# Performance work log

Hardware: AMD Instinct MI355X
Metric: run time of the kernel (lower is better)

The kernel has to match this reference:

```python
import jax, jax.numpy as jnp
import numpy as np

B, N, P, DIM, H = 8, 1024, 77, 1024, 16
HD = DIM // H
LN_EPS = 1e-5


def setup_inputs() -> dict:
    key = jax.random.key(0)
    ks = jax.random.split(key, 8)
    s = 0.02  # weight init scale
    return {
        "x": jax.random.normal(ks[0], (B, N, DIM), jnp.float32),
        "x_text": jax.random.normal(ks[1], (B, P, DIM), jnp.float32),
        "Wq": jax.random.normal(ks[2], (DIM, DIM), jnp.float32) * s,
        "Wk": jax.random.normal(ks[3], (DIM, DIM), jnp.float32) * s,
        "Wv": jax.random.normal(ks[4], (DIM, DIM), jnp.float32) * s,
        "gate": jax.random.normal(ks[5], (1, H, 1, 1), jnp.float32) * 0.5,
        "ln_g": jnp.ones((DIM,), jnp.float32),
        "ln_b": jnp.zeros((DIM,), jnp.float32),
        "Wp": jax.random.normal(ks[6], (DIM, DIM), jnp.float32) * s,
        "bp": jnp.zeros((DIM,), jnp.float32),
    }


def reference(x, x_text, Wq, Wk, Wv, gate, ln_g, ln_b, Wp, bp):
    b, n, c = x.shape
    h = gate.shape[1]
    # subln projections; prefix text tokens are concatenated onto k/v (not q)
    q = x @ Wq.T                                             # [B,N,C]
    k = jnp.concatenate([x_text @ Wk.T, x @ Wk.T], axis=1)   # [B,P+N,C]
    v = jnp.concatenate([x_text @ Wv.T, x @ Wv.T], axis=1)   # [B,P+N,C]
    kv = k.shape[1]
    q = q.reshape(b, n, h, -1).transpose(0, 2, 1, 3)         # [B,H,N,d]
    k = k.reshape(b, kv, h, -1).transpose(0, 2, 1, 3)        # [B,H,K,d]
    v = v.reshape(b, kv, h, -1).transpose(0, 2, 1, 3)        # [B,H,K,d]
    d = q.shape[-1]
    scores = jnp.einsum('bhnd,bhkd->bhnk', q, k) / jnp.sqrt(jnp.float32(d))
    # gated split softmax: first key column is softmaxed alone (== 1) and gated
    first = jnp.tanh(gate) * jnp.ones_like(scores[..., :1])  # [B,H,N,1]
    rest = jax.nn.softmax(scores[..., 1:], axis=-1)          # [B,H,N,K-1]
    attn = jnp.concatenate([first, rest], axis=-1)           # [B,H,N,K]
    out = jnp.einsum('bhnk,bhkd->bhnd', attn, v)             # AV reduce
    out = out.transpose(0, 2, 1, 3).reshape(b, n, -1)        # [B,N,C]
    # original casts to bfloat16 then back to LN weight dtype
    out = out.astype(jnp.bfloat16).astype(jnp.float32)
    mu = jnp.mean(out, axis=-1, keepdims=True)
    var = jnp.var(out, axis=-1, keepdims=True)
    out = (out - mu) / jnp.sqrt(var + LN_EPS) * ln_g + ln_b
    return out @ Wp.T + bp
```

## Files before the change

kernel.cpp:

```cpp
#include <hip/hip_runtime.h>
#include <stdint.h>

#define DIM   1024
#define NB    8
#define NSEQ  1024
#define NP    77
#define NH    16
#define NKVR  1104
#define KVP   1104
#define QSCALE 0.18033688011112042f

typedef short          bf16x8 __attribute__((ext_vector_type(8)));
typedef float          f32x4  __attribute__((ext_vector_type(4)));
typedef float          f32x16 __attribute__((ext_vector_type(16)));
typedef unsigned short u16x8  __attribute__((ext_vector_type(8)));
typedef unsigned short u16x4  __attribute__((ext_vector_type(4)));
typedef unsigned int   u32x4  __attribute__((ext_vector_type(4)));

__device__ __forceinline__ float bf2f(unsigned short h) {
  return __uint_as_float(((unsigned int)h) << 16);
}
__device__ __forceinline__ unsigned short f2bf(float f) {
  unsigned int u = __float_as_uint(f);
  unsigned int r = u + 0x7FFFu + ((u >> 16) & 1u);
  return (unsigned short)(r >> 16);
}
__device__ __forceinline__ unsigned int cvt_pk_bf16(float lo, float hi) {
  unsigned int r;
  asm volatile("v_cvt_pk_bf16_f32 %0, %1, %2" : "=v"(r) : "v"(lo), "v"(hi));
  return r;
}

__global__ __launch_bounds__(256) void cast_kernel(const float* __restrict__ in,
                                                   unsigned short* __restrict__ out,
                                                   int n4, float scale) {
  int i = blockIdx.x * 256 + threadIdx.x;
  if (i >= n4) return;
  float4 v = reinterpret_cast<const float4*>(in)[i];
  u16x4 o;
  o[0] = f2bf(v.x * scale); o[1] = f2bf(v.y * scale);
  o[2] = f2bf(v.z * scale); o[3] = f2bf(v.w * scale);
  reinterpret_cast<u16x4*>(out)[i] = o;
}

__global__ __launch_bounds__(256) void cast_x_kernel(const float* __restrict__ in,
                                                     unsigned short* __restrict__ xkv) {
  int i = blockIdx.x * 256 + threadIdx.x;
  if (i >= (NB * NSEQ * DIM) / 4) return;
  const int e    = i * 4;
  const int row  = e >> 10;
  const int cin  = e & 1023;
  const int batch = row >> 10;
  const int r     = row & 1023;
  float4 v = *reinterpret_cast<const float4*>(in + (size_t)e);
  u16x4 o;
  o[0] = f2bf(v.x); o[1] = f2bf(v.y); o[2] = f2bf(v.z); o[3] = f2bf(v.w);
  *reinterpret_cast<u16x4*>(xkv + (size_t)(batch * NKVR + 80 + r) * DIM + cin) = o;
}

__global__ __launch_bounds__(256) void cast_xt_kernel(const float* __restrict__ in,
                                                      unsigned short* __restrict__ xkv) {
  int i = blockIdx.x * 256 + threadIdx.x;
  if (i >= (NB * NP * DIM) / 4) return;
  const int e    = i * 4;
  const int row  = e >> 10;
  const int cin  = e & 1023;
  const int batch = row / NP;
  const int r     = row - batch * NP;
  float4 v = *reinterpret_cast<const float4*>(in + (size_t)e);
  u16x4 o;
  o[0] = f2bf(v.x); o[1] = f2bf(v.y); o[2] = f2bf(v.z); o[3] = f2bf(v.w);
  *reinterpret_cast<u16x4*>(xkv + (size_t)(batch * NKVR + r) * DIM + cin) = o;
}

__global__ __launch_bounds__(256) void zero_hole_kernel(unsigned short* __restrict__ xkv) {
  int i = blockIdx.x * 256 + threadIdx.x;
  if (i >= (NB * 3 * DIM) / 4) return;
  const int e    = i * 4;
  const int row  = e >> 10;
  const int cin  = e & 1023;
  const int batch = row / 3;
  const int hr    = row - batch * 3;
  u16x4 z = {0, 0, 0, 0};
  *reinterpret_cast<u16x4*>(xkv + (size_t)(batch * NKVR + 77 + hr) * DIM + cin) = z;
}

__device__ __forceinline__ void gload_lds16(const void* g, void* l) {
  __builtin_amdgcn_global_load_lds(
      (const __attribute__((address_space(1))) void*)g,
      (__attribute__((address_space(3))) void*)l, 16, 0, 0);
}

__global__ __launch_bounds__(256) void gemm_qkv(
    const unsigned short* __restrict__ A, const unsigned short* __restrict__ B,
    unsigned short* __restrict__ Qo, unsigned short* __restrict__ Ko,
    unsigned short* __restrict__ Vto) {
  __shared__ __align__(16) unsigned short As[128 * 32];
  __shared__ __align__(16) unsigned short Bs[128 * 32];
  const int id   = blockIdx.x;
  const int sid  = (id & 7) * 207 + (id >> 3);
  const int bx   = sid / 24;
  const int by   = sid - bx * 24;
  const int m0   = bx * 128;
  const int n0   = by * 128;
  const int t    = threadIdx.x;
  const int w    = t >> 6;
  const int lane = t & 63;
  const int wr   = w >> 1, wc = w & 1;
  const int lr   = lane & 15;
  const int k0   = (lane >> 4) * 8;

  f32x4 acc[4][4];
#pragma unroll
  for (int i = 0; i < 4; ++i)
#pragma unroll
    for (int j = 0; j < 4; ++j) acc[i][j] = f32x4{0.f, 0.f, 0.f, 0.f};

  for (int kt = 0; kt < 32; ++kt) {
#pragma unroll
    for (int p = 0; p < 2; ++p) {
      const int c   = p * 256 + t;
      const int row = c >> 2;
      const int cid = c & 3;
      gload_lds16(A + (size_t)(m0 + row) * DIM + kt * 32 + cid * 8,
                  (char*)As + p * 4096 + w * 1024);
      gload_lds16(B + (size_t)(n0 + row) * DIM + kt * 32 + cid * 8,
                  (char*)Bs + p * 4096 + w * 1024);
    }
    __syncthreads();
    bf16x8 af[4], bfr[4];
#pragma unroll
    for (int mi = 0; mi < 4; ++mi)
      af[mi] = *reinterpret_cast<const bf16x8*>(As + (wr * 64 + mi * 16 + lr) * 32 + k0);
#pragma unroll
    for (int ni = 0; ni < 4; ++ni)
      bfr[ni] = *reinterpret_cast<const bf16x8*>(Bs + (wc * 64 + ni * 16 + lr) * 32 + k0);
#pragma unroll
    for (int mi = 0; mi < 4; ++mi)
#pragma unroll
      for (int ni = 0; ni < 4; ++ni)
        acc[mi][ni] = __builtin_amdgcn_mfma_f32_16x16x32_bf16(af[mi], bfr[ni], acc[mi][ni], 0, 0, 0);
    __syncthreads();
  }

  const int rq  = lane >> 4;
  const int seg = n0 >> 10;
  if (seg == 0) {
#pragma unroll
    for (int mi = 0; mi < 4; ++mi) {
#pragma unroll
      for (int i = 0; i < 4; ++i) {
        const int m     = m0 + wr * 64 + mi * 16 + rq * 4 + i;
        const int batch = m / NKVR;
        const int kv    = m - batch * NKVR;
        if (kv < 80) continue;
        const size_t qrow = (size_t)batch * NSEQ + (kv - 80);
#pragma unroll
        for (int ni = 0; ni < 4; ++ni) {
          const int col = n0 + wc * 64 + ni * 16 + lr;
          Qo[qrow * DIM + col] = f2bf(acc[mi][ni][i]);
        }
      }
    }
  } else if (seg == 1) {
#pragma unroll
    for (int mi = 0; mi < 4; ++mi) {
#pragma unroll
      for (int i = 0; i < 4; ++i) {
        const int m = m0 + wr * 64 + mi * 16 + rq * 4 + i;
#pragma unroll
        for (int ni = 0; ni < 4; ++ni) {
          const int col = n0 + wc * 64 + ni * 16 + lr - 1024;
          Ko[(size_t)m * DIM + col] = f2bf(acc[mi][ni][i]);
        }
      }
    }
  } else {
#pragma unroll
    for (int mi = 0; mi < 4; ++mi) {
      const int mb    = m0 + wr * 64 + mi * 16 + rq * 4;
      const int batch = mb / NKVR;
      const int kv    = mb - batch * NKVR;
#pragma unroll
      for (int ni = 0; ni < 4; ++ni) {
        const int col = n0 + wc * 64 + ni * 16 + lr - 2048;
        const int hh = col >> 6, dd = col & 63;
        u16x4 o;
        o[0] = f2bf(acc[mi][ni][0]); o[1] = f2bf(acc[mi][ni][1]);
        o[2] = f2bf(acc[mi][ni][2]); o[3] = f2bf(acc[mi][ni][3]);
        *reinterpret_cast<u16x4*>(Vto +
            ((size_t)((batch * NH + hh) * 64 + dd)) * KVP + kv) = o;
      }
    }
  }
}

__global__ __launch_bounds__(256) void gemm_out(
    const unsigned short* __restrict__ A, const unsigned short* __restrict__ B,
    float* __restrict__ C, const float* __restrict__ bias) {
  __shared__ __align__(16) unsigned short As[128 * 32];
  __shared__ __align__(16) unsigned short Bs[128 * 32];
  const int t    = threadIdx.x;
  const int w    = t >> 6;
  const int lane = t & 63;
  const int m0   = blockIdx.x * 128;
  const int n0   = blockIdx.y * 128;
  const int wr   = w >> 1, wc = w & 1;
  const int lr   = lane & 15;
  const int k0   = (lane >> 4) * 8;

  f32x4 acc[4][4];
#pragma unroll
  for (int i = 0; i < 4; ++i)
#pragma unroll
    for (int j = 0; j < 4; ++j) acc[i][j] = f32x4{0.f, 0.f, 0.f, 0.f};

  for (int kt = 0; kt < 32; ++kt) {
#pragma unroll
    for (int p = 0; p < 2; ++p) {
      const int c   = p * 256 + t;
      const int row = c >> 2;
      const int cid = c & 3;
      gload_lds16(A + (size_t)(m0 + row) * DIM + kt * 32 + cid * 8,
                  (char*)As + p * 4096 + w * 1024);
      gload_lds16(B + (size_t)(n0 + row) * DIM + kt * 32 + cid * 8,
                  (char*)Bs + p * 4096 + w * 1024);
    }
    __syncthreads();
    bf16x8 af[4], bfr[4];
#pragma unroll
    for (int mi = 0; mi < 4; ++mi)
      af[mi] = *reinterpret_cast<const bf16x8*>(As + (wr * 64 + mi * 16 + lr) * 32 + k0);
#pragma unroll
    for (int ni = 0; ni < 4; ++ni)
      bfr[ni] = *reinterpret_cast<const bf16x8*>(Bs + (wc * 64 + ni * 16 + lr) * 32 + k0);
#pragma unroll
    for (int mi = 0; mi < 4; ++mi)
#pragma unroll
      for (int ni = 0; ni < 4; ++ni)
        acc[mi][ni] = __builtin_amdgcn_mfma_f32_16x16x32_bf16(af[mi], bfr[ni], acc[mi][ni], 0, 0, 0);
    __syncthreads();
  }

  const int rq = lane >> 4;
#pragma unroll
  for (int mi = 0; mi < 4; ++mi) {
#pragma unroll
    for (int i = 0; i < 4; ++i) {
      const int m = m0 + wr * 64 + mi * 16 + rq * 4 + i;
#pragma unroll
      for (int ni = 0; ni < 4; ++ni) {
        const int col = n0 + wc * 64 + ni * 16 + lr;
        C[(size_t)m * DIM + col] = acc[mi][ni][i] + bias[col];
      }
    }
  }
}

__global__ __launch_bounds__(128, 4) void attn_mfma(
    const unsigned short* __restrict__ Q, const unsigned short* __restrict__ K,
    const unsigned short* __restrict__ Vt, const float* __restrict__ gate,
    unsigned short* __restrict__ O) {
  const int wid  = threadIdx.x >> 6;
  const int lane = threadIdx.x & 63;
  const int ql   = lane & 31;
  const int hi   = lane >> 5;
  const int bh   = blockIdx.x;
  const int b    = bh >> 4;
  const int h    = bh & 15;
  const int q0   = blockIdx.y * 64 + wid * 32;

  __shared__ float v0f[2][64];

  const unsigned short* Vtbase = Vt + ((size_t)((b * NH + h) * 64)) * KVP;
  const unsigned short* Kbase  = K  + ((size_t)b * NKVR) * DIM + h * 64 + hi * 8;

  v0f[wid][lane] = bf2f(Vtbase[(size_t)lane * KVP]);

  bf16x8 bq[4];
  const unsigned short* Qrow = Q + ((size_t)(b * NSEQ + q0 + ql)) * DIM + h * 64 + hi * 8;
#pragma unroll
  for (int j = 0; j < 4; ++j)
    bq[j] = *reinterpret_cast<const bf16x8*>(Qrow + j * 16);

  f32x16 o0, o1;
#pragma unroll
  for (int r = 0; r < 16; ++r) { o0[r] = 0.f; o1[r] = 0.f; }
  float lsum = 0.f;

  auto kblock = [&](int kbase, int mm) {
    int krow = kbase + ql;
    if (mm == 3) krow = krow < NKVR ? krow : (NKVR - 1);
    const unsigned short* kr = Kbase + (size_t)krow * DIM;
    bf16x8 ak[4];
#pragma unroll
    for (int j = 0; j < 4; ++j)
      ak[j] = *reinterpret_cast<const bf16x8*>(kr + j * 16);

    f32x16 s;
#pragma unroll
    for (int r = 0; r < 16; ++r) s[r] = 0.f;
#pragma unroll
    for (int j = 0; j < 4; ++j)
      s = __builtin_amdgcn_mfma_f32_32x32x16_bf16(ak[j], bq[j], s, 0, 0, 0);

    bf16x8 av[2][2];
#pragma unroll
    for (int ss = 0; ss < 2; ++ss) {
      if (mm == 3 && ss == 1) continue;
      const int kv = kbase + ss * 16 + hi * 8;
#pragma unroll
      for (int n = 0; n < 2; ++n)
        av[ss][n] = *reinterpret_cast<const bf16x8*>(
            Vtbase + (size_t)(n * 32 + ql) * KVP + kv);
    }

    if (mm == 1) {
      if (hi == 0) s[0] = -1.0e30f;
    } else if (mm == 2) {
      if (hi == 1) { s[5] = -1.0e30f; s[6] = -1.0e30f; s[7] = -1.0e30f; }
    } else if (mm == 3) {
#pragma unroll
      for (int r = 8; r < 16; ++r) s[r] = -1.0e30f;
    }

    float ts = 0.f;
#pragma unroll
    for (int r = 0; r < 16; ++r) { s[r] = __builtin_exp2f(s[r]); ts += s[r]; }
    lsum += ts;

#pragma unroll
    for (int ss = 0; ss < 2; ++ss) {
      if (mm == 3 && ss == 1) continue;
      const int R = 8 * ss;
      const unsigned int p0 = cvt_pk_bf16(s[R + 0], s[R + 1]);
      const unsigned int p1 = cvt_pk_bf16(s[R + 2], s[R + 3]);
      const unsigned int p2 = cvt_pk_bf16(s[R + 4], s[R + 5]);
      const unsigned int p3 = cvt_pk_bf16(s[R + 6], s[R + 7]);
      const unsigned int t0 = (unsigned int)__shfl_xor((int)p0, 32);
      const unsigned int t1 = (unsigned int)__shfl_xor((int)p1, 32);
      const unsigned int t2 = (unsigned int)__shfl_xor((int)p2, 32);
      const unsigned int t3 = (unsigned int)__shfl_xor((int)p3, 32);
      u32x4 wv;
      wv[0] = hi ? t2 : p0;
      wv[1] = hi ? t3 : p1;
      wv[2] = hi ? p2 : t0;
      wv[3] = hi ? p3 : t1;
      const bf16x8 bp = __builtin_bit_cast(bf16x8, wv);
      o0 = __builtin_amdgcn_mfma_f32_32x32x16_bf16(av[ss][0], bp, o0, 0, 0, 0);
      o1 = __builtin_amdgcn_mfma_f32_32x32x16_bf16(av[ss][1], bp, o1, 0, 0, 0);
    }
  };

  kblock(0, 1);
  kblock(32, 0);
  kblock(64, 2);
  kblock(96, 0);
  for (int t = 2; t < 17; ++t) {
    kblock(t * 64, 0);
    kblock(t * 64 + 32, 0);
  }
  kblock(1088, 3);

  const float lt  = lsum + __shfl_xor(lsum, 32);
  const float inv = 1.f / lt;
  const float gv  = tanhf(gate[h]);
  unsigned short* Orow = O + ((size_t)(b * NSEQ + q0 + ql)) * DIM + h * 64;
#pragma unroll
  for (int n = 0; n < 2; ++n) {
#pragma unroll
    for (int g = 0; g < 4; ++g) {
      const int d0 = n * 32 + 8 * g + 4 * hi;
      const float4 vv = *reinterpret_cast<const float4*>(&v0f[wid][d0]);
      float e0, e1, e2, e3;
      if (n == 0) {
        e0 = o0[4 * g + 0]; e1 = o0[4 * g + 1]; e2 = o0[4 * g + 2]; e3 = o0[4 * g + 3];
      } else {
        e0 = o1[4 * g + 0]; e1 = o1[4 * g + 1]; e2 = o1[4 * g + 2]; e3 = o1[4 * g + 3];
      }
      u16x4 ov;
      ov[0] = f2bf(e0 * inv + gv * vv.x);
      ov[1] = f2bf(e1 * inv + gv * vv.y);
      ov[2] = f2bf(e2 * inv + gv * vv.z);
      ov[3] = f2bf(e3 * inv + gv * vv.w);
      *reinterpret_cast<u16x4*>(Orow + d0) = ov;
    }
  }
}

__global__ __launch_bounds__(256) void ln_kernel(const unsigned short* __restrict__ in,
                                                 const float* __restrict__ g,
                                                 const float* __restrict__ beta,
                                                 unsigned short* __restrict__ out) {
  const int row = blockIdx.x;
  const int t   = threadIdx.x;
  const u16x4 hv = *reinterpret_cast<const u16x4*>(in + (size_t)row * DIM + t * 4);
  const float v0 = bf2f(hv[0]), v1 = bf2f(hv[1]), v2 = bf2f(hv[2]), v3 = bf2f(hv[3]);
  float sum = v0 + v1 + v2 + v3;
  float sq  = v0 * v0 + v1 * v1 + v2 * v2 + v3 * v3;
  for (int off = 32; off; off >>= 1) {
    sum += __shfl_xor(sum, off);
    sq  += __shfl_xor(sq, off);
  }
  __shared__ float red[8];
  if ((t & 63) == 0) { red[t >> 6] = sum; red[4 + (t >> 6)] = sq; }
  __syncthreads();
  sum = red[0] + red[1] + red[2] + red[3];
  sq  = red[4] + red[5] + red[6] + red[7];
  const float mu  = sum * (1.f / DIM);
  const float var = sq * (1.f / DIM) - mu * mu;
  const float rs  = 1.f / sqrtf(var + 1e-5f);
  const float4 gv = *reinterpret_cast<const float4*>(g + t * 4);
  const float4 bv = *reinterpret_cast<const float4*>(beta + t * 4);
  u16x4 o;
  o[0] = f2bf((v0 - mu) * rs * gv.x + bv.x);
  o[1] = f2bf((v1 - mu) * rs * gv.y + bv.y);
  o[2] = f2bf((v2 - mu) * rs * gv.z + bv.z);
  o[3] = f2bf((v3 - mu) * rs * gv.w + bv.w);
  *reinterpret_cast<u16x4*>(out + (size_t)row * DIM + t * 4) = o;
}

extern "C" void kernel_launch(void* const* d_in, const int* in_sizes, int n_in,
                              void* d_out, int out_size, void* d_ws, size_t ws_size,
                              hipStream_t stream) {
  const float* x    = (const float*)d_in[0];
  const float* xt   = (const float*)d_in[1];
  const float* Wq   = (const float*)d_in[2];
  const float* Wk   = (const float*)d_in[3];
  const float* Wv   = (const float*)d_in[4];
  const float* gate = (const float*)d_in[5];
  const float* lng  = (const float*)d_in[6];
  const float* lnbt = (const float*)d_in[7];
  const float* Wp   = (const float*)d_in[8];
  const float* bp   = (const float*)d_in[9];

  char* ws = (char*)d_ws;
  unsigned short* xkvb = (unsigned short*)(ws + 0);
  unsigned short* Wqkv = (unsigned short*)(ws + 18087936);
  unsigned short* Qb   = (unsigned short*)(ws + 24379392);
  unsigned short* Kb   = (unsigned short*)(ws + 41156608);
  unsigned short* Vtb  = (unsigned short*)(ws + 59244544);
  unsigned short* attnb = xkvb;
  unsigned short* lnob  = Qb;
  unsigned short* Wpb   = Wqkv;

  cast_x_kernel<<<dim3((NB * NSEQ * DIM / 4 + 255) / 256), 256, 0, stream>>>(x, xkvb);
  cast_xt_kernel<<<dim3((NB * NP * DIM / 4 + 255) / 256), 256, 0, stream>>>(xt, xkvb);
  zero_hole_kernel<<<dim3((NB * 3 * DIM / 4 + 255) / 256), 256, 0, stream>>>(xkvb);
  const int w4 = DIM * DIM / 4;
  cast_kernel<<<dim3((w4 + 255) / 256), 256, 0, stream>>>(Wq, Wqkv, w4, QSCALE);
  cast_kernel<<<dim3((w4 + 255) / 256), 256, 0, stream>>>(Wk, Wqkv + DIM * DIM, w4, 1.0f);
  cast_kernel<<<dim3((w4 + 255) / 256), 256, 0, stream>>>(Wv, Wqkv + 2 * DIM * DIM, w4, 1.0f);

  gemm_qkv<<<dim3(69 * 24), 256, 0, stream>>>(xkvb, Wqkv, Qb, Kb, Vtb);

  attn_mfma<<<dim3(128, 16), 128, 0, stream>>>(Qb, Kb, Vtb, gate, attnb);

  cast_kernel<<<dim3((w4 + 255) / 256), 256, 0, stream>>>(Wp, Wpb, w4, 1.0f);
  ln_kernel<<<dim3(NB * NSEQ), 256, 0, stream>>>(attnb, lng, lnbt, lnob);
  gemm_out<<<dim3(64, 8), 256, 0, stream>>>(lnob, Wpb, (float*)d_out, bp);
}
```

Measured before the change: 260.5 us.

## Double-buffer K fragment loads and stage attention output through LDS

Splits the attention inner block into a K-load step and a compute body, so the next K tile is prefetched into alternating register buffers while the current tile's MFMAs and softmax run. This hides global load latency. The epilogue now writes output fragments into a padded LDS tile and then stores full 16-byte rows, making the global writes coalesced. The cost is higher register pressure from the second K buffer, which may reduce occupancy, plus an extra LDS round trip and a barrier.

```diff
diff --git a/kernel.cpp b/kernel.cpp
--- a/kernel.cpp
+++ b/kernel.cpp
@@ -271,6 +271,7 @@
   const int q0   = blockIdx.y * 64 + wid * 32;
 
   __shared__ float v0f[2][64];
+  __shared__ __align__(16) unsigned short o_lds[2][32 * 72];
 
   const unsigned short* Vtbase = Vt + ((size_t)((b * NH + h) * 64)) * KVP;
   const unsigned short* Kbase  = K  + ((size_t)b * NKVR) * DIM + h * 64 + hi * 8;
@@ -288,15 +289,17 @@
   for (int r = 0; r < 16; ++r) { o0[r] = 0.f; o1[r] = 0.f; }
   float lsum = 0.f;
 
-  auto kblock = [&](int kbase, int mm) {
+  auto load_k = [&](int kbase, bf16x8 (&ak)[4]) {
     int krow = kbase + ql;
-    if (mm == 3) krow = krow < NKVR ? krow : (NKVR - 1);
+    krow = krow < NKVR ? krow : (NKVR - 1);
     const unsigned short* kr = Kbase + (size_t)krow * DIM;
-    bf16x8 ak[4];
 #pragma unroll
     for (int j = 0; j < 4; ++j)
       ak[j] = *reinterpret_cast<const bf16x8*>(kr + j * 16);
-
+  };
+
+  auto body = [&](int kbase, int mm, bf16x8 (&ak)[4],
+                  bool pf, int nkbase, bf16x8 (&nak)[4]) {
     f32x16 s;
 #pragma unroll
     for (int r = 0; r < 16; ++r) s[r] = 0.f;
@@ -304,16 +307,18 @@
     for (int j = 0; j < 4; ++j)
       s = __builtin_amdgcn_mfma_f32_32x32x16_bf16(ak[j], bq[j], s, 0, 0, 0);
 
-    bf16x8 av[2][2];
-#pragma unroll
-    for (int ss = 0; ss < 2; ++ss) {
-      if (mm == 3 && ss == 1) continue;
-      const int kv = kbase + ss * 16 + hi * 8;
+    bf16x8 av0[2], av1[2];
+#pragma unroll
+    for (int n = 0; n < 2; ++n)
+      av0[n] = *reinterpret_cast<const bf16x8*>(
+          Vtbase + (size_t)(n * 32 + ql) * KVP + kbase + hi * 8);
+    if (mm != 3) {
 #pragma unroll
       for (int n = 0; n < 2; ++n)
-        av[ss][n] = *reinterpret_cast<const bf16x8*>(
-            Vtbase + (size_t)(n * 32 + ql) * KVP + kv);
-    }
+        av1[n] = *reinterpret_cast<const bf16x8*>(
+            Vtbase + (size_t)(n * 32 + ql) * KVP + kbase + 16 + hi * 8);
+    }
+    if (pf) load_k(nkbase, nak);
 
     if (mm == 1) {
       if (hi == 0) s[0] = -1.0e30f;
@@ -329,14 +334,11 @@
     for (int r = 0; r < 16; ++r) { s[r] = __builtin_exp2f(s[r]); ts += s[r]; }
     lsum += ts;
 
-#pragma unroll
-    for (int ss = 0; ss < 2; ++ss) {
-      if (mm == 3 && ss == 1) continue;
-      const int R = 8 * ss;
-      const unsigned int p0 = cvt_pk_bf16(s[R + 0], s[R + 1]);
-      const unsigned int p1 = cvt_pk_bf16(s[R + 2], s[R + 3]);
-      const unsigned int p2 = cvt_pk_bf16(s[R + 4], s[R + 5]);
-      const unsigned int p3 = cvt_pk_bf16(s[R + 6], s[R + 7]);
+    {
+      const unsigned int p0 = cvt_pk_bf16(s[0], s[1]);
+      const unsigned int p1 = cvt_pk_bf16(s[2], s[3]);
+      const unsigned int p2 = cvt_pk_bf16(s[4], s[5]);
+      const unsigned int p3 = cvt_pk_bf16(s[6], s[7]);
       const unsigned int t0 = (unsigned int)__shfl_xor((int)p0, 32);
       const unsigned int t1 = (unsigned int)__shfl_xor((int)p1, 32);
       const unsigned int t2 = (unsigned int)__shfl_xor((int)p2, 32);
@@ -347,31 +349,50 @@
       wv[2] = hi ? p2 : t0;
       wv[3] = hi ? p3 : t1;
       const bf16x8 bp = __builtin_bit_cast(bf16x8, wv);
-      o0 = __builtin_amdgcn_mfma_f32_32x32x16_bf16(av[ss][0], bp, o0, 0, 0, 0);
-      o1 = __builtin_amdgcn_mfma_f32_32x32x16_bf16(av[ss][1], bp, o1, 0, 0, 0);
+      o0 = __builtin_amdgcn_mfma_f32_32x32x16_bf16(av0[0], bp, o0, 0, 0, 0);
+      o1 = __builtin_amdgcn_mfma_f32_32x32x16_bf16(av0[1], bp, o1, 0, 0, 0);
+    }
+    if (mm != 3) {
+      const unsigned int p0 = cvt_pk_bf16(s[8],  s[9]);
+      const unsigned int p1 = cvt_pk_bf16(s[10], s[11]);
+      const unsigned int p2 = cvt_pk_bf16(s[12], s[13]);
+      const unsigned int p3 = cvt_pk_bf16(s[14], s[15]);
+      const unsigned int t0 = (unsigned int)__shfl_xor((int)p0, 32);
+      const unsigned int t1 = (unsigned int)__shfl_xor((int)p1, 32);
+      const unsigned int t2 = (unsigned int)__shfl_xor((int)p2, 32);
+      const unsigned int t3 = (unsigned int)__shfl_xor((int)p3, 32);
+      u32x4 wv;
+      wv[0] = hi ? t2 : p0;
+      wv[1] = hi ? t3 : p1;
+      wv[2] = hi ? p2 : t0;
+      wv[3] = hi ? p3 : t1;
+      const bf16x8 bp = __builtin_bit_cast(bf16x8, wv);
+      o0 = __builtin_amdgcn_mfma_f32_32x32x16_bf16(av1[0], bp, o0, 0, 0, 0);
+      o1 = __builtin_amdgcn_mfma_f32_32x32x16_bf16(av1[1], bp, o1, 0, 0, 0);
     }
   };
 
-  kblock(0, 1);
-  kblock(32, 0);
-  kblock(64, 2);
-  kblock(96, 0);
-  for (int t = 2; t < 17; ++t) {
-    kblock(t * 64, 0);
-    kblock(t * 64 + 32, 0);
-  }
-  kblock(1088, 3);
+  bf16x8 akA[4], akB[4];
+  load_k(0, akA);
+  body(0,  1, akA, true, 32,  akB);
+  body(32, 0, akB, true, 64,  akA);
+  body(64, 2, akA, true, 96,  akB);
+  body(96, 0, akB, true, 128, akA);
+  for (int i = 4; i < 34; i += 2) {
+    body(32 * i,       0, akA, true, 32 * (i + 1), akB);
+    body(32 * (i + 1), 0, akB, true, 32 * (i + 2), akA);
+  }
+  body(1088, 3, akA, false, 0, akB);
 
   const float lt  = lsum + __shfl_xor(lsum, 32);
   const float inv = 1.f / lt;
   const float gv  = tanhf(gate[h]);
-  unsigned short* Orow = O + ((size_t)(b * NSEQ + q0 + ql)) * DIM + h * 64;
 #pragma unroll
   for (int n = 0; n < 2; ++n) {
 #pragma unroll
     for (int g = 0; g < 4; ++g) {
-      const int d0 = n * 32 + 8 * g + 4 * hi;
-      const float4 vv = *reinterpret_cast<const float4*>(&v0f[wid][d0]);
+      const int col = n * 32 + 8 * g + 4 * hi;
+      const float4 vv = *reinterpret_cast<const float4*>(&v0f[wid][col]);
       float e0, e1, e2, e3;
       if (n == 0) {
         e0 = o0[4 * g + 0]; e1 = o0[4 * g + 1]; e2 = o0[4 * g + 2]; e3 = o0[4 * g + 3];
@@ -383,8 +404,18 @@
       ov[1] = f2bf(e1 * inv + gv * vv.y);
       ov[2] = f2bf(e2 * inv + gv * vv.z);
       ov[3] = f2bf(e3 * inv + gv * vv.w);
-      *reinterpret_cast<u16x4*>(Orow + d0) = ov;
-    }
+      *reinterpret_cast<u16x4*>(&o_lds[wid][ql * 72 + col]) = ov;
+    }
+  }
+  __syncthreads();
+  unsigned short* Obase = O + ((size_t)(b * NSEQ + q0)) * DIM + h * 64;
+  const int rr = lane >> 3;
+  const int cc = lane & 7;
+#pragma unroll
+  for (int it = 0; it < 4; ++it) {
+    const int row = it * 8 + rr;
+    const u16x8 v8 = *reinterpret_cast<const u16x8*>(&o_lds[wid][row * 72 + cc * 8]);
+    *reinterpret_cast<u16x8*>(Obase + (size_t)row * DIM + cc * 8) = v8;
   }
 }
 
```

Measured after the change: 271.5 us. 1.04x slower.
